# Kernel optimization log

Measured on AMD Instinct MI355X. Metric: run time of the kernel, lower is better.

Reference implementation:

```python
import jax, jax.numpy as jnp
import numpy as np

N_NODES = 50000
N_EDGES = 800000
NUM_FEATURES = 128
H1, H2, H3 = 256, 512, 256


def setup_inputs() -> dict:
    key = jax.random.key(0)
    ks = jax.random.split(key, 14)

    def lin(kw, fan_in, fan_out):
        # torch nn.Linear-style init, stored as [in, out] for x @ W
        bound = 1.0 / np.sqrt(fan_in)
        W = jax.random.uniform(kw, (fan_in, fan_out), jnp.float32, -bound, bound)
        b = jnp.zeros((fan_out,), jnp.float32)
        return W, b

    x = jax.random.normal(ks[0], (N_NODES, NUM_FEATURES), jnp.float32)
    edge_index = jax.random.randint(ks[1], (2, N_EDGES), 0, N_NODES, jnp.int64 if jax.config.jax_enable_x64 else jnp.int32)

    W1, b1 = lin(ks[2], NUM_FEATURES, H1)
    W2, b2 = lin(ks[3], H1, H2)
    W3, b3 = lin(ks[4], H2, H3)
    Wf1, bf1 = lin(ks[5], H3, 128)
    Wf2, bf2 = lin(ks[6], 128, 64)
    Wf3, bf3 = lin(ks[7], 64, 1)

    return {"x": x, "edge_index": edge_index,
            "W1": W1, "b1": b1, "W2": W2, "b2": b2, "W3": W3, "b3": b3,
            "Wf1": Wf1, "bf1": bf1, "Wf2": Wf2, "bf2": bf2, "Wf3": Wf3, "bf3": bf3}


def gcn_conv(x, W, b, row, col, dinv_row_col, n):
    # PyG GCNConv: out = D^{-1/2} (A+I) D^{-1/2} (x W) + b, self-loops already in row/col
    h = x @ W                              # [N, out]
    msg = h[row] * dinv_row_col[:, None]   # gather + edge-wise scale: [E+N, out]
    return jax.ops.segment_sum(msg, col, num_segments=n) + b


def reference(x, edge_index, W1, b1, W2, b2, W3, b3, Wf1, bf1, Wf2, bf2, Wf3, bf3):
    n = x.shape[0]
    loop = jnp.arange(n, dtype=edge_index.dtype)
    row = jnp.concatenate([edge_index[0], loop])   # sources (with self-loops)
    col = jnp.concatenate([edge_index[1], loop])   # targets (with self-loops)

    # symmetric normalization (computed once; identical for all three convs)
    deg = jax.ops.segment_sum(jnp.ones(col.shape[0], x.dtype), col, num_segments=n)
    dinv = jnp.where(deg > 0, jax.lax.rsqrt(deg), 0.0)
    norm = dinv[row] * dinv[col]                   # [E+N]

    h = jax.nn.relu(gcn_conv(x, W1, b1, row, col, norm, n))
    h = jax.nn.relu(gcn_conv(h, W2, b2, row, col, norm, n))
    h = jax.nn.relu(gcn_conv(h, W3, b3, row, col, norm, n))

    g = jnp.mean(h, axis=0, keepdims=True)         # [1, H3]
    g = jax.nn.relu(g @ Wf1 + bf1)
    g = jax.nn.relu(g @ Wf2 + bf2)
    return g @ Wf3 + bf3                           # [1, 1]
```

## Files before the change

kernel.cpp:

```cpp
#include <hip/hip_runtime.h>
#include <hip/hip_bf16.h>

#define N_NODES 50000
#define N_EDGES 800000
#define N_BUCKETS 64
#define M_PAD 50048

#define NS 8
#define SLICE_DIV 6250
#define NC (N_NODES * NS)
#define AGG_BLOCKS 1024
#define DPW 13
#define INIT_NB ((NC + 255) / 256)
#define SCAN2_NB ((NC + 1023) / 1024)

typedef short short8 __attribute__((ext_vector_type(8)));
typedef float floatx4 __attribute__((ext_vector_type(4)));
typedef float floatx2 __attribute__((ext_vector_type(2)));

__device__ __forceinline__ unsigned short f2bf(float f) {
    unsigned u = __float_as_uint(f);
    unsigned r = (u + 0x7fff + ((u >> 16) & 1)) >> 16;
    return (unsigned short)r;
}
__device__ __forceinline__ float bf2f(unsigned short h) {
    return __uint_as_float(((unsigned)h) << 16);
}
__device__ __forceinline__ void expand2(unsigned u, float& lo, float& hi) {
    lo = __uint_as_float(u << 16);
    hi = __uint_as_float(u & 0xffff0000u);
}

__device__ __forceinline__ unsigned pack4_fp8(float f0, float f1, float f2, float f3) {
    int v = __builtin_amdgcn_cvt_pk_fp8_f32(f0, f1, 0, false);
    v = __builtin_amdgcn_cvt_pk_fp8_f32(f2, f3, v, true);
    return (unsigned)v;
}
__device__ __forceinline__ void accum_fp8x4(float* a, unsigned u, float w) {
    floatx2 lo = __builtin_amdgcn_cvt_pk_f32_fp8((int)u, false);
    floatx2 hi = __builtin_amdgcn_cvt_pk_f32_fp8((int)u, true);
    a[0] += lo[0] * w; a[1] += lo[1] * w;
    a[2] += hi[0] * w; a[3] += hi[1] * w;
}
__device__ __forceinline__ void accum_fp8x2(float* a, unsigned u, float w) {
    floatx2 lo = __builtin_amdgcn_cvt_pk_f32_fp8((int)u, false);
    a[0] += lo[0] * w; a[1] += lo[1] * w;
}

__device__ __forceinline__ void gload16(const void* gp, void* lp) {
    __builtin_amdgcn_global_load_lds(
        (const __attribute__((address_space(1))) unsigned int*)gp,
        (__attribute__((address_space(3))) unsigned int*)lp,
        16, 0, 0);
}

__global__ void k_init2(int* __restrict__ cnt2, float* __restrict__ gb) {
    int i = blockIdx.x * blockDim.x + threadIdx.x;
    if (i < NC) {
        int s = i / N_NODES;
        int v = i - s * N_NODES;
        cnt2[i] = (s == v / SLICE_DIV) ? 1 : 0;
    }
    if (i < N_BUCKETS * 256) gb[i] = 0.0f;
}

__global__ void k_count2(const int* __restrict__ row, const int* __restrict__ col,
                         int* __restrict__ cnt2) {
    int e = blockIdx.x * blockDim.x + threadIdx.x;
    if (e >= N_EDGES) return;
    int s = row[e] / SLICE_DIV;
    atomicAdd(&cnt2[s * N_NODES + col[e]], 1);
}

__global__ void k_dinv(const int* __restrict__ cnt2, float* __restrict__ dinv) {
    int v = blockIdx.x * blockDim.x + threadIdx.x;
    if (v >= N_NODES) return;
    int c = 0;
#pragma unroll
    for (int s = 0; s < NS; ++s) c += cnt2[s * N_NODES + v];
    dinv[v] = 1.0f / sqrtf((float)c);
}

__global__ __launch_bounds__(256) void k_scanA2(const int* __restrict__ cnt2,
                                                int* __restrict__ bsum) {
    __shared__ int red[256];
    int t = threadIdx.x;
    int base = blockIdx.x * 1024 + t * 4;
    int sum = 0;
    if (base + 3 < NC) {
        int4 c = *(const int4*)&cnt2[base];
        sum = c.x + c.y + c.z + c.w;
    } else {
#pragma unroll
        for (int k = 0; k < 4; ++k)
            if (base + k < NC) sum += cnt2[base + k];
    }
    red[t] = sum;
    __syncthreads();
    for (int d = 128; d > 0; d >>= 1) {
        if (t < d) red[t] += red[t + d];
        __syncthreads();
    }
    if (t == 0) bsum[blockIdx.x] = red[0];
}

__global__ __launch_bounds__(512) void k_scanB2(const int* __restrict__ bsum,
                                                int* __restrict__ bbase) {
    __shared__ int sc[512];
    int t = threadIdx.x;
    int v = (t < SCAN2_NB) ? bsum[t] : 0;
    sc[t] = v;
    __syncthreads();
    for (int d = 1; d < 512; d <<= 1) {
        int x = 0;
        if (t >= d) x = sc[t - d];
        __syncthreads();
        if (t >= d) sc[t] += x;
        __syncthreads();
    }
    if (t < SCAN2_NB) bbase[t] = sc[t] - v;
}

__global__ __launch_bounds__(256) void k_scanC2(const int* __restrict__ cnt2,
                                                const int* __restrict__ bbase,
                                                int* __restrict__ off2,
                                                int* __restrict__ cursor2) {
    __shared__ int sc[256];
    int t = threadIdx.x;
    int base = blockIdx.x * 1024 + t * 4;
    int c0 = 0, c1 = 0, c2 = 0, c3 = 0;
    if (base + 3 < NC) {
        int4 c = *(const int4*)&cnt2[base];
        c0 = c.x; c1 = c.y; c2 = c.z; c3 = c.w;
    } else {
        if (base     < NC) c0 = cnt2[base];
        if (base + 1 < NC) c1 = cnt2[base + 1];
        if (base + 2 < NC) c2 = cnt2[base + 2];
        if (base + 3 < NC) c3 = cnt2[base + 3];
    }
    int tsum = c0 + c1 + c2 + c3;
    sc[t] = tsum;
    __syncthreads();
    for (int d = 1; d < 256; d <<= 1) {
        int x = 0;
        if (t >= d) x = sc[t - d];
        __syncthreads();
        if (t >= d) sc[t] += x;
        __syncthreads();
    }
    int tex = sc[t] - tsum + bbase[blockIdx.x];
    int e0 = tex, e1 = tex + c0, e2 = e1 + c1, e3 = e2 + c2;
    if (base     < NC) { off2[base]     = e0; cursor2[base]     = e0; }
    if (base + 1 < NC) { off2[base + 1] = e1; cursor2[base + 1] = e1; }
    if (base + 2 < NC) { off2[base + 2] = e2; cursor2[base + 2] = e2; }
    if (base + 3 == NC - 1) off2[NC] = e3 + c3;
    if (base + 3 < NC) { off2[base + 3] = e3; cursor2[base + 3] = e3; }
}

__global__ void k_fill2(const int* __restrict__ row, const int* __restrict__ col,
                        const float* __restrict__ dinv, int* __restrict__ cursor2,
                        int2* __restrict__ epack) {
    int e = blockIdx.x * blockDim.x + threadIdx.x;
    if (e < N_EDGES) {
        int r = row[e];
        int s = r / SLICE_DIV;
        int p = atomicAdd(&cursor2[s * N_NODES + col[e]], 1);
        epack[p] = make_int2(r, __float_as_int(dinv[r]));
    }
    if (e < N_NODES) {
        int s = e / SLICE_DIV;
        int p = atomicAdd(&cursor2[s * N_NODES + e], 1);
        epack[p] = make_int2(e, __float_as_int(dinv[e]));
    }
}

__global__ void k_prepW(const float* __restrict__ W,
                        unsigned short* __restrict__ Th,
                        unsigned short* __restrict__ Tl, int K, int N) {
    int idx = blockIdx.x * blockDim.x + threadIdx.x;
    if (idx >= K * N) return;
    int n = idx / K, k = idx - n * K;
    float v = W[(size_t)k * N + n];
    unsigned short h = f2bf(v);
    Th[idx] = h;
    Tl[idx] = f2bf(v - bf2f(h));
}

__global__ void k_prepX8(const float* __restrict__ x, unsigned char* __restrict__ xq) {
    int i = blockIdx.x * blockDim.x + threadIdx.x;
    if (i >= N_NODES * 32) return;
    const float* s = x + (size_t)i * 4;
    *(unsigned*)&xq[(size_t)i * 4] = pack4_fp8(s[0], s[1], s[2], s[3]);
}

template <int DIM, int POOL>
__global__ __launch_bounds__(256) void k_aggp(
    const unsigned char* __restrict__ xq, const int* __restrict__ off2,
    const int2* __restrict__ epack, const float* __restrict__ dinv,
    const float* __restrict__ bias, unsigned short* __restrict__ outb,
    float* __restrict__ gb) {
    const int FPL = DIM / 64;
    const int TABLE_BYTES = N_NODES * DIM;
    const int SLICE_BYTES = SLICE_DIV * DIM;
    const int CA  = (DIM == 256) ? 12512 : 6256;
    const int PFL = (DIM == 256) ? 4 : 2;
    const int wv = __builtin_amdgcn_readfirstlane(threadIdx.x >> 6);
    const int li = threadIdx.x & 63;
    const int wid = blockIdx.x * 4 + wv;
    const int d0 = wid * DPW;
    const int lblk = blockIdx.x >> 3;
    const unsigned char* __restrict__ xl = xq + li * FPL;

    float acc[DPW][FPL];
#pragma unroll
    for (int di = 0; di < DPW; ++di)
#pragma unroll
        for (int i = 0; i < FPL; ++i) acc[di][i] = 0.0f;

    {
        uint4 pf[4];
        int base = lblk * CA + threadIdx.x * 16;
#pragma unroll
        for (int i = 0; i < PFL; ++i) {
            int q = base + i * 4096;
            q = q > TABLE_BYTES - 16 ? TABLE_BYTES - 16 : q;
            pf[i] = *(const uint4*)(xq + q);
        }
#pragma unroll
        for (int i = 0; i < PFL; ++i)
            asm volatile("" ::"v"(pf[i].x), "v"(pf[i].y), "v"(pf[i].z), "v"(pf[i].w));
    }

    for (int s = 0; s < NS; ++s) {
        int cur[DPW], end[DPW];
        int rounds = 0;
#pragma unroll
        for (int di = 0; di < DPW; ++di) {
            int v = d0 + di;
            int vc = (v < N_NODES) ? v : (N_NODES - 1);
            int cell = s * N_NODES + vc;
            int jb = off2[cell];
            int je = (v < N_NODES) ? off2[cell + 1] : jb;
            cur[di] = jb;
            end[di] = je;
            rounds = max(rounds, je - jb);
        }

        uint4 pf[4];
        const bool have_pf = (s + 1 < NS);
        if (have_pf) {
            int base = (s + 1) * SLICE_BYTES + lblk * CA + threadIdx.x * 16;
#pragma unroll
            for (int i = 0; i < PFL; ++i) {
                int q = base + i * 4096;
                q = q > TABLE_BYTES - 16 ? TABLE_BYTES - 16 : q;
                pf[i] = *(const uint4*)(xq + q);
            }
        }

        for (int r = 0; r < rounds; ++r) {
#pragma unroll
            for (int di = 0; di < DPW; ++di) {
                bool act = cur[di] < end[di];
                int jj = act ? cur[di] : (end[di] - 1);
                jj = jj < 0 ? 0 : jj;
                int2 ed = epack[jj];
                float w = act ? __int_as_float(ed.y) : 0.0f;
                cur[di]++;
                if constexpr (DIM == 256) {
                    unsigned gv = *(const unsigned*)&xl[(size_t)ed.x * DIM];
                    accum_fp8x4(acc[di], gv, w);
                } else {
                    unsigned gv = (unsigned)*(const unsigned short*)&xl[(size_t)ed.x * DIM];
                    accum_fp8x2(acc[di], gv, w);
                }
            }
        }

        if (have_pf) {
#pragma unroll
            for (int i = 0; i < PFL; ++i)
                asm volatile("" ::"v"(pf[i].x), "v"(pf[i].y), "v"(pf[i].z), "v"(pf[i].w));
        }
    }

    if constexpr (!POOL) {
#pragma unroll
        for (int di = 0; di < DPW; ++di) {
            int v = d0 + di;
            if (v >= N_NODES) continue;
            float dv = dinv[v];
            if constexpr (DIM == 256) {
                uint2 o;
                o.x = (unsigned)f2bf(acc[di][0] * dv) | ((unsigned)f2bf(acc[di][1] * dv) << 16);
                o.y = (unsigned)f2bf(acc[di][2] * dv) | ((unsigned)f2bf(acc[di][3] * dv) << 16);
                *(uint2*)&outb[(size_t)v * DIM + li * 4] = o;
            } else {
                unsigned o = (unsigned)f2bf(acc[di][0] * dv) | ((unsigned)f2bf(acc[di][1] * dv) << 16);
                *(unsigned*)&outb[(size_t)v * DIM + li * 2] = o;
            }
        }
    } else {
        floatx4 bv = *(const floatx4*)&bias[li * 4];
        float ps0 = 0.f, ps1 = 0.f, ps2 = 0.f, ps3 = 0.f;
#pragma unroll
        for (int di = 0; di < DPW; ++di) {
            int v = d0 + di;
            if (v >= N_NODES) continue;
            float dv = dinv[v];
            ps0 += fmaxf(acc[di][0] * dv + bv[0], 0.0f);
            ps1 += fmaxf(acc[di][1] * dv + bv[1], 0.0f);
            ps2 += fmaxf(acc[di][2] * dv + bv[2], 0.0f);
            ps3 += fmaxf(acc[di][3] * dv + bv[3], 0.0f);
        }
        float* g0 = &gb[(wid & (N_BUCKETS - 1)) * 256 + li * 4];
        atomicAdd(g0 + 0, ps0);
        atomicAdd(g0 + 1, ps1);
        atomicAdd(g0 + 2, ps2);
        atomicAdd(g0 + 3, ps3);
    }
}

template <int BIAS, int RELU, int OUTFP8>
__global__ __launch_bounds__(256) void k_gemm_b(
    const unsigned short* __restrict__ A,
    const unsigned short* __restrict__ Bh, const unsigned short* __restrict__ Bl,
    const float* __restrict__ bias, void* __restrict__ Cout,
    int M, int K, int N) {
    __shared__ unsigned short smem[4 * 4096];
    unsigned short* As  = smem;
    unsigned short* BsH = smem + 4096;
    unsigned short* BsL = smem + 8192;
    int tid = threadIdx.x;
    int lane = tid & 63;
    int w = tid >> 6;
    int wr = w & 1, wc = w >> 1;
    int bm = blockIdx.x * 128, bn = blockIdx.y * 128;

    floatx4 acc[4][4];
    floatx4 zero = {0.f, 0.f, 0.f, 0.f};
#pragma unroll
    for (int t = 0; t < 4; ++t)
#pragma unroll
        for (int u = 0; u < 4; ++u) acc[t][u] = zero;

    int c0 = w * 2, c1 = c0 + 1;
    int srow = lane >> 2;
    int kg = ((lane & 3) - ((lane >> 3) & 3)) & 3;
    int kc = kg * 8;
    const unsigned short* Ap0 = A + (size_t)(bm + c0 * 16 + srow) * K + kc;
    const unsigned short* Ap1 = A + (size_t)(bm + c1 * 16 + srow) * K + kc;
    const unsigned short* Bh0 = Bh + (size_t)(bn + c0 * 16 + srow) * K + kc;
    const unsigned short* Bh1 = Bh + (size_t)(bn + c1 * 16 + srow) * K + kc;
    const unsigned short* Bl0 = Bl + (size_t)(bn + c0 * 16 + srow) * K + kc;
    const unsigned short* Bl1 = Bl + (size_t)(bn + c1 * 16 + srow) * K + kc;

    const int KT = K >> 5;
    int fr = lane & 15;
    int fq = lane >> 4;
    int cl = ((fq + (fr >> 1)) & 3) * 8;

    for (int kt = 0; kt < KT; ++kt) {
        int k0 = kt * 32;
        gload16(Ap0 + k0, As + c0 * 512);
        gload16(Ap1 + k0, As + c1 * 512);
        gload16(Bh0 + k0, BsH + c0 * 512);
        gload16(Bh1 + k0, BsH + c1 * 512);
        gload16(Bl0 + k0, BsL + c0 * 512);
        gload16(Bl1 + k0, BsL + c1 * 512);
        __syncthreads();
        short8 av[4], bhv[4], blv[4];
#pragma unroll
        for (int t = 0; t < 4; ++t) {
            av[t]  = *(const short8*)&As[(wr * 64 + t * 16 + fr) * 32 + cl];
            bhv[t] = *(const short8*)&BsH[(wc * 64 + t * 16 + fr) * 32 + cl];
            blv[t] = *(const short8*)&BsL[(wc * 64 + t * 16 + fr) * 32 + cl];
        }
#pragma unroll
        for (int t = 0; t < 4; ++t)
#pragma unroll
            for (int u = 0; u < 4; ++u) {
                acc[t][u] = __builtin_amdgcn_mfma_f32_16x16x32_bf16(av[t], bhv[u], acc[t][u], 0, 0, 0);
                acc[t][u] = __builtin_amdgcn_mfma_f32_16x16x32_bf16(av[t], blv[u], acc[t][u], 0, 0, 0);
            }
        __syncthreads();
    }

    unsigned short* cq = smem + w * 4096;
#pragma unroll
    for (int u = 0; u < 4; ++u) {
        int colq = u * 16 + fr;
        float bv = BIAS ? bias[bn + wc * 64 + colq] : 0.0f;
#pragma unroll
        for (int t = 0; t < 4; ++t) {
#pragma unroll
            for (int r = 0; r < 4; ++r) {
                float o = acc[t][u][r] + bv;
                if (RELU) o = fmaxf(o, 0.f);
                cq[(t * 16 + fq * 4 + r) * 64 + colq] = f2bf(o);
            }
        }
    }
    __syncthreads();
    int lr = tid >> 4;
    int lc = (tid & 15) * 8;
    int wcq = lc >> 6;
    int lcq = lc & 63;
#pragma unroll
    for (int i = 0; i < 8; ++i) {
        int rowt = i * 16 + lr;
        int wrq = rowt >> 6;
        const unsigned short* src =
            smem + (wrq + wcq * 2) * 4096 + (rowt & 63) * 64 + lcq;
        int rowg = bm + rowt;
        if (rowg < M) {
            if (!OUTFP8) {
                unsigned short* C = (unsigned short*)Cout;
                *(uint4*)&C[(size_t)rowg * N + bn + lc] = *(const uint4*)src;
            } else {
                uint4 b = *(const uint4*)src;
                float f0, f1, f2, f3, f4, f5, f6, f7;
                expand2(b.x, f0, f1); expand2(b.y, f2, f3);
                expand2(b.z, f4, f5); expand2(b.w, f6, f7);
                uint2 q;
                q.x = pack4_fp8(f0, f1, f2, f3);
                q.y = pack4_fp8(f4, f5, f6, f7);
                unsigned char* C8 = (unsigned char*)Cout;
                *(uint2*)&C8[(size_t)rowg * N + bn + lc] = q;
            }
        }
    }
}

__global__ void k_mlp(const float* __restrict__ gb,
                      const float* __restrict__ Wf1, const float* __restrict__ bf1,
                      const float* __restrict__ Wf2, const float* __restrict__ bf2,
                      const float* __restrict__ Wf3, const float* __restrict__ bf3,
                      float* __restrict__ out) {
    __shared__ float s0[256], s1[128], s2[64];
    int t = threadIdx.x;
    float sum = 0.0f;
    for (int b = 0; b < N_BUCKETS; ++b) sum += gb[b * 256 + t];
    s0[t] = sum * (1.0f / (float)N_NODES);
    __syncthreads();
    if (t < 128) {
        float a = bf1[t];
        for (int k = 0; k < 256; ++k) a += s0[k] * Wf1[k * 128 + t];
        s1[t] = fmaxf(a, 0.0f);
    }
    __syncthreads();
    if (t < 64) {
        float a = bf2[t];
        for (int k = 0; k < 128; ++k) a += s1[k] * Wf2[k * 64 + t];
        s2[t] = fmaxf(a, 0.0f);
    }
    __syncthreads();
    if (t == 0) {
        float a = bf3[0];
        for (int k = 0; k < 64; ++k) a += s2[k] * Wf3[k];
        out[0] = a;
    }
}

extern "C" void kernel_launch(void* const* d_in, const int* in_sizes, int n_in,
                              void* d_out, int out_size, void* d_ws, size_t ws_size,
                              hipStream_t stream) {
    const float* x  = (const float*)d_in[0];
    const int* ei   = (const int*)d_in[1];
    const float* W1 = (const float*)d_in[2];
    const float* b1 = (const float*)d_in[3];
    const float* W2 = (const float*)d_in[4];
    const float* b2 = (const float*)d_in[5];
    const float* W3 = (const float*)d_in[6];
    const float* b3 = (const float*)d_in[7];
    const float* Wf1 = (const float*)d_in[8];
    const float* bf1 = (const float*)d_in[9];
    const float* Wf2 = (const float*)d_in[10];
    const float* bf2 = (const float*)d_in[11];
    const float* Wf3 = (const float*)d_in[12];
    const float* bf3 = (const float*)d_in[13];
    float* out = (float*)d_out;

    char* p = (char*)d_ws;
    auto alloc = [&](size_t bytes) {
        void* r = (void*)p;
        p += (bytes + 255) & ~((size_t)255);
        return r;
    };
    int*   cnt2    = (int*)  alloc((size_t)NC * sizeof(int));
    int*   off2    = (int*)  alloc((size_t)(NC + 1) * sizeof(int));
    int*   cursor2 = (int*)  alloc((size_t)NC * sizeof(int));
    int*   bsum2   = (int*)  alloc(SCAN2_NB * sizeof(int));
    int*   bbase2  = (int*)  alloc(SCAN2_NB * sizeof(int));
    float* dinv    = (float*)alloc(N_NODES * sizeof(float));
    int2*  epack   = (int2*) alloc((size_t)(N_EDGES + N_NODES) * sizeof(int2));
    float* gb      = (float*)alloc(N_BUCKETS * 256 * sizeof(float));
    unsigned short* W1h = (unsigned short*)alloc(128 * 256 * 2);
    unsigned short* W1l = (unsigned short*)alloc(128 * 256 * 2);
    unsigned short* W2h = (unsigned short*)alloc(256 * 512 * 2);
    unsigned short* W2l = (unsigned short*)alloc(256 * 512 * 2);
    unsigned short* W3h = (unsigned short*)alloc(512 * 256 * 2);
    unsigned short* W3l = (unsigned short*)alloc(512 * 256 * 2);
    unsigned char*  xq  = (unsigned char*) alloc((size_t)N_NODES * 128);
    unsigned short* t0  = (unsigned short*)alloc((size_t)M_PAD * 128 * 2);
    unsigned char*  h1q = (unsigned char*) alloc((size_t)N_NODES * 256);
    unsigned short* t1  = (unsigned short*)alloc((size_t)M_PAD * 256 * 2);
    unsigned short* h2  = (unsigned short*)alloc((size_t)M_PAD * 512 * 2);
    unsigned char*  t2q = (unsigned char*) alloc((size_t)N_NODES * 256);

    const int* row = ei;
    const int* col = ei + N_EDGES;

    const int NB = (N_NODES + 255) / 256;
    const int EB = (N_EDGES + 255) / 256;

    k_init2<<<INIT_NB, 256, 0, stream>>>(cnt2, gb);
    k_count2<<<EB, 256, 0, stream>>>(row, col, cnt2);
    k_dinv<<<NB, 256, 0, stream>>>(cnt2, dinv);
    k_scanA2<<<SCAN2_NB, 256, 0, stream>>>(cnt2, bsum2);
    k_scanB2<<<1, 512, 0, stream>>>(bsum2, bbase2);
    k_scanC2<<<SCAN2_NB, 256, 0, stream>>>(cnt2, bbase2, off2, cursor2);
    k_fill2<<<EB, 256, 0, stream>>>(row, col, dinv, cursor2, epack);

    k_prepW<<<(128 * 256 + 255) / 256, 256, 0, stream>>>(W1, W1h, W1l, 128, 256);
    k_prepW<<<(256 * 512 + 255) / 256, 256, 0, stream>>>(W2, W2h, W2l, 256, 512);
    k_prepW<<<(512 * 256 + 255) / 256, 256, 0, stream>>>(W3, W3h, W3l, 512, 256);
    k_prepX8<<<(N_NODES * 32 + 255) / 256, 256, 0, stream>>>(x, xq);

    const int M = N_NODES;
    const int MB = (M + 127) / 128;

    k_aggp<128, 0><<<AGG_BLOCKS, 256, 0, stream>>>(
        xq, off2, epack, dinv, nullptr, t0, nullptr);
    {
        dim3 grid(MB, 256 / 128);
        k_gemm_b<1, 1, 1><<<grid, 256, 0, stream>>>(t0, W1h, W1l, b1, h1q, M, 128, 256);
    }
    k_aggp<256, 0><<<AGG_BLOCKS, 256, 0, stream>>>(
        h1q, off2, epack, dinv, nullptr, t1, nullptr);
    {
        dim3 grid(MB, 512 / 128);
        k_gemm_b<1, 1, 0><<<grid, 256, 0, stream>>>(t1, W2h, W2l, b2, h2, M, 256, 512);
    }
    {
        dim3 grid(MB, 256 / 128);
        k_gemm_b<0, 0, 1><<<grid, 256, 0, stream>>>(h2, W3h, W3l, nullptr, t2q, M, 512, 256);
    }
    k_aggp<256, 1><<<AGG_BLOCKS, 256, 0, stream>>>(
        t2q, off2, epack, dinv, b3, nullptr, gb);

    k_mlp<<<1, 256, 0, stream>>>(gb, Wf1, bf1, Wf2, bf2, Wf3, bf3, out);
}
```

Baseline: 549.6 us.

## Add per-XCD spin barriers between source slices in aggregation kernels

Adds a software barrier, built on atomics with a bounded spin, among the blocks that share an XCD (blockIdx mod 8). It runs after the initial L2 prefetch and after each source-slice phase of the aggregation kernel, so all blocks on an XCD work on the same slice of the feature table at once and keep it resident in that XCD's L2. It also sets launch_bounds min-blocks to 4 so all 1024 blocks can be co-resident. The spin adds latency, and its correctness relies on co-residency and on the assumed round-robin block-to-XCD mapping. The bounded spin count prevents deadlock but can let blocks run ahead out of step.

```diff
diff --git a/kernel.cpp b/kernel.cpp
--- a/kernel.cpp
+++ b/kernel.cpp
@@ -13,6 +13,9 @@
 #define DPW 13
 #define INIT_NB ((NC + 255) / 256)
 #define SCAN2_NB ((NC + 1023) / 1024)
+#define NXCD 8
+#define XBLK (AGG_BLOCKS / NXCD)
+#define BAR_STRIDE 128
 
 typedef short short8 __attribute__((ext_vector_type(8)));
 typedef float floatx4 __attribute__((ext_vector_type(4)));
@@ -54,7 +57,22 @@
         16, 0, 0);
 }
 
-__global__ void k_init2(int* __restrict__ cnt2, float* __restrict__ gb) {
+__device__ __forceinline__ void xcd_barrier(int* __restrict__ bar, int slot) {
+    __syncthreads();
+    if (threadIdx.x == 0) {
+        int* p = bar + slot;
+        atomicAdd(p, 1);
+        int it = 0;
+        while (atomicAdd(p, 0) < XBLK && it < 6000) {
+            ++it;
+            __builtin_amdgcn_s_sleep(4);
+        }
+    }
+    __syncthreads();
+}
+
+__global__ void k_init2(int* __restrict__ cnt2, float* __restrict__ gb,
+                        int* __restrict__ bar) {
     int i = blockIdx.x * blockDim.x + threadIdx.x;
     if (i < NC) {
         int s = i / N_NODES;
@@ -62,6 +80,7 @@
         cnt2[i] = (s == v / SLICE_DIV) ? 1 : 0;
     }
     if (i < N_BUCKETS * 256) gb[i] = 0.0f;
+    if (i < 3 * BAR_STRIDE) bar[i] = 0;
 }
 
 __global__ void k_count2(const int* __restrict__ row, const int* __restrict__ col,
@@ -194,11 +213,11 @@
 }
 
 template <int DIM, int POOL>
-__global__ __launch_bounds__(256) void k_aggp(
+__global__ __launch_bounds__(256, 4) void k_aggp(
     const unsigned char* __restrict__ xq, const int* __restrict__ off2,
     const int2* __restrict__ epack, const float* __restrict__ dinv,
     const float* __restrict__ bias, unsigned short* __restrict__ outb,
-    float* __restrict__ gb) {
+    float* __restrict__ gb, int* __restrict__ bar) {
     const int FPL = DIM / 64;
     const int TABLE_BYTES = N_NODES * DIM;
     const int SLICE_BYTES = SLICE_DIV * DIM;
@@ -209,6 +228,7 @@
     const int wid = blockIdx.x * 4 + wv;
     const int d0 = wid * DPW;
     const int lblk = blockIdx.x >> 3;
+    int* __restrict__ mybar = bar + (blockIdx.x & (NXCD - 1)) * 16;
     const unsigned char* __restrict__ xl = xq + li * FPL;
 
     float acc[DPW][FPL];
@@ -230,6 +250,7 @@
         for (int i = 0; i < PFL; ++i)
             asm volatile("" ::"v"(pf[i].x), "v"(pf[i].y), "v"(pf[i].z), "v"(pf[i].w));
     }
+    xcd_barrier(mybar, 0);
 
     for (int s = 0; s < NS; ++s) {
         int cur[DPW], end[DPW];
@@ -281,6 +302,7 @@
 #pragma unroll
             for (int i = 0; i < PFL; ++i)
                 asm volatile("" ::"v"(pf[i].x), "v"(pf[i].y), "v"(pf[i].z), "v"(pf[i].w));
+            xcd_barrier(mybar, s + 1);
         }
     }
 
@@ -493,6 +515,7 @@
     int*   bsum2   = (int*)  alloc(SCAN2_NB * sizeof(int));
     int*   bbase2  = (int*)  alloc(SCAN2_NB * sizeof(int));
     float* dinv    = (float*)alloc(N_NODES * sizeof(float));
+    int*   bar     = (int*)  alloc(3 * BAR_STRIDE * sizeof(int));
     int2*  epack   = (int2*) alloc((size_t)(N_EDGES + N_NODES) * sizeof(int2));
     float* gb      = (float*)alloc(N_BUCKETS * 256 * sizeof(float));
     unsigned short* W1h = (unsigned short*)alloc(128 * 256 * 2);
@@ -514,7 +537,7 @@
     const int NB = (N_NODES + 255) / 256;
     const int EB = (N_EDGES + 255) / 256;
 
-    k_init2<<<INIT_NB, 256, 0, stream>>>(cnt2, gb);
+    k_init2<<<INIT_NB, 256, 0, stream>>>(cnt2, gb, bar);
     k_count2<<<EB, 256, 0, stream>>>(row, col, cnt2);
     k_dinv<<<NB, 256, 0, stream>>>(cnt2, dinv);
     k_scanA2<<<SCAN2_NB, 256, 0, stream>>>(cnt2, bsum2);
@@ -531,13 +554,13 @@
     const int MB = (M + 127) / 128;
 
     k_aggp<128, 0><<<AGG_BLOCKS, 256, 0, stream>>>(
-        xq, off2, epack, dinv, nullptr, t0, nullptr);
+        xq, off2, epack, dinv, nullptr, t0, nullptr, bar);
     {
         dim3 grid(MB, 256 / 128);
         k_gemm_b<1, 1, 1><<<grid, 256, 0, stream>>>(t0, W1h, W1l, b1, h1q, M, 128, 256);
     }
     k_aggp<256, 0><<<AGG_BLOCKS, 256, 0, stream>>>(
-        h1q, off2, epack, dinv, nullptr, t1, nullptr);
+        h1q, off2, epack, dinv, nullptr, t1, nullptr, bar + BAR_STRIDE);
     {
         dim3 grid(MB, 512 / 128);
         k_gemm_b<1, 1, 0><<<grid, 256, 0, stream>>>(t1, W2h, W2l, b2, h2, M, 256, 512);
@@ -547,7 +570,7 @@
         k_gemm_b<0, 0, 1><<<grid, 256, 0, stream>>>(h2, W3h, W3l, nullptr, t2q, M, 512, 256);
     }
     k_aggp<256, 1><<<AGG_BLOCKS, 256, 0, stream>>>(
-        t2q, off2, epack, dinv, b3, nullptr, gb);
+        t2q, off2, epack, dinv, b3, nullptr, gb, bar + 2 * BAR_STRIDE);
 
     k_mlp<<<1, 256, 0, stream>>>(gb, Wf1, bf1, Wf2, bf2, Wf3, bf3, out);
 }
```

After: 880.6 us. 1.6x slower.
